# Kernel optimization log

Hardware: AMD Instinct MI355X
Metric: run time of the kernel (lower is better)

Reference implementation:

```python
import jax, jax.numpy as jnp
import numpy as np

K = 16          # neighboursnum
NEG_SLOPE = 0.01  # torch LeakyReLU default
EPS = 1e-5      # torch BatchNorm default


def _bn(x, gamma, beta, axes):
    # BatchNorm in training mode: biased batch stats over `axes`, channel dim = 1
    mu = x.mean(axes, keepdims=True)
    var = x.var(axes, keepdims=True)
    shape = [1] * x.ndim
    shape[1] = -1
    return (x - mu) / jnp.sqrt(var + EPS) * gamma.reshape(shape) + beta.reshape(shape)


def _lrelu(x):
    return jnp.where(x >= 0, x, NEG_SLOPE * x)


def setup_inputs() -> dict:
    key = jax.random.key(0)
    ks = jax.random.split(key, 9)
    B, D, N, O = 4, 64, 4096, 128
    s = 0.05
    return {
        "f_in": jax.random.normal(ks[0], (B, D, N), jnp.float32),
        "w_local": jax.random.normal(ks[1], (O, 2 * D + 1), jnp.float32) * s,
        "g_local": jnp.ones((O,), jnp.float32),
        "b_local": jnp.zeros((O,), jnp.float32),
        "w_sem": jax.random.normal(ks[2], (O, D), jnp.float32) * s,
        "g_sem": jnp.ones((O,), jnp.float32),
        "b_sem": jnp.zeros((O,), jnp.float32),
        "w_full": jax.random.normal(ks[3], (O, 2 * O), jnp.float32) * s,
        "g_full": jnp.ones((O,), jnp.float32),
        "b_full": jnp.zeros((O,), jnp.float32),
        "wq": jax.random.normal(ks[4], (D, D), jnp.float32) * s,
        "bq": jax.random.normal(ks[5], (D,), jnp.float32) * s,
        "wk": jax.random.normal(ks[6], (D, D), jnp.float32) * s,
        "bk": jax.random.normal(ks[7], (D,), jnp.float32) * s,
        "wv": jax.random.normal(ks[8], (D, D), jnp.float32) * s,
        "bv": jax.random.normal(jax.random.fold_in(key, 99), (D,), jnp.float32) * s,
    }


def reference(f_in, w_local, g_local, b_local, w_sem, g_sem, b_sem,
              w_full, g_full, b_full, wq, bq, wk, bk, wv, bv):
    B, D, N = f_in.shape
    # --- knn on feature space: pairwise negative squared distance, topk ---
    xx = jnp.sum(f_in * f_in, axis=1)                       # (B,N)
    inner = jnp.einsum('bdm,bdn->bmn', f_in, f_in)          # (B,N,N)
    pd = -xx[:, :, None] + 2.0 * inner - xx[:, None, :]     # -||xi-xj||^2
    idx = jax.lax.top_k(pd, K)[1]                           # (B,N,K) nearest
    # --- gather graph feature ---
    x_t = jnp.swapaxes(f_in, 1, 2)                          # (B,N,D)
    neigh = x_t[jnp.arange(B)[:, None, None], idx]          # (B,N,K,D)
    central = jnp.broadcast_to(x_t[:, :, None, :], neigh.shape)
    dist = jnp.linalg.norm(neigh - central, axis=3, keepdims=True)  # (B,N,K,1)
    feat = jnp.concatenate([central, neigh, dist], axis=3)  # (B,N,K,2D+1)
    feat = jnp.transpose(feat, (0, 3, 1, 2))                # (B,2D+1,N,K)
    # --- localConv (1x1 conv2d, no bias) + BN2d + LeakyReLU, max over K ---
    intra = _lrelu(_bn(jnp.einsum('oc,bcnk->bonk', w_local, feat),
                       g_local, b_local, (0, 2, 3)))
    intra = intra.max(axis=-1)                              # (B,O,N)
    # --- self-attention over points ---
    q = jnp.einsum('od,bdn->bon', wq, f_in) + bq[None, :, None]
    k = jnp.einsum('od,bdn->bon', wk, f_in) + bk[None, :, None]
    v = jnp.einsum('od,bdn->bon', wv, f_in) + bv[None, :, None]
    scores = jax.nn.softmax(
        jnp.einsum('bdm,bdn->bmn', q, k) / jnp.sqrt(jnp.float32(D)), axis=-1)
    fgt = jnp.einsum('bmn,bdn->bdm', scores, v)             # (B,D,N)
    # --- semConv (1x1 conv1d) + BN1d + LeakyReLU ---
    inter = _lrelu(_bn(jnp.einsum('od,bdn->bon', w_sem, fgt),
                       g_sem, b_sem, (0, 2)))               # (B,O,N)
    # --- fullConv on concat ---
    cat = jnp.concatenate([intra, inter], axis=1)           # (B,2O,N)
    out = _lrelu(_bn(jnp.einsum('oc,bcn->bon', w_full, cat),
                     g_full, b_full, (0, 2)))               # (B,O,N)
    return out
```

## Files before the change

kernel.cpp:

```cpp
#include <hip/hip_runtime.h>
#include <math.h>

constexpr int NB = 4;
constexpr int ND = 64;
constexpr int NNN = 4096;
constexpr int NO = 128;
constexpr int NK = 16;
constexpr float NEG = 0.01f;
constexpr float BN_EPS = 1e-5f;

typedef unsigned short u16;
typedef unsigned int u32;
typedef __attribute__((ext_vector_type(8))) short short8;
typedef __attribute__((ext_vector_type(4))) float floatx4;

constexpr int OFF_XX    = 0;
constexpr int OFF_IDX   = 16384;
constexpr int OFF_D2    = 278528;
constexpr int OFF_Q     = 540672;
constexpr int OFF_K     = 1589248;
constexpr int OFF_V     = 2637824;
constexpr int OFF_FGT   = 3686400;
constexpr int OFF_APRE  = 4734976;
constexpr int OFF_BPRE  = 6832128;
constexpr int OFF_IMAX  = 8929280;
constexpr int OFF_IMIN  = 11026432;
constexpr int OFF_ZSEM  = OFF_Q;
constexpr int OFF_ZFULL = OFF_V;
constexpr int OFF_STATS = 13123584;
constexpr int OFF_COEF  = 13124352;
constexpr int OFF_LINV  = 13125120;

__device__ __forceinline__ u16 f2b(float x) {
  u32 u = __builtin_bit_cast(u32, x);
  u += 0x7fffu + ((u >> 16) & 1u);
  return (u16)(u >> 16);
}

template <int CTRL>
__device__ __forceinline__ float fmax_dpp(float v) {
  int b = __builtin_bit_cast(int, v);
  int s = __builtin_amdgcn_update_dpp(b, b, CTRL, 0xF, 0xF, false);
  return fmaxf(v, __builtin_bit_cast(float, s));
}
__device__ __forceinline__ void pairmax(float av, int ai, float bv, int bi, float& rv, int& ri) {
  bool tk = bv > av;
  rv = tk ? bv : av;
  ri = tk ? bi : ai;
}

__global__ void k_xx(const float* __restrict__ f, float* __restrict__ xx) {
  int gid = blockIdx.x * 256 + threadIdx.x;
  int b = gid >> 12, n = gid & 4095;
  const float* fb = f + b * ND * NNN + n;
  float s = 0.f;
#pragma unroll
  for (int d = 0; d < ND; ++d) { float v = fb[d * NNN]; s += v * v; }
  xx[gid] = s;
}

__global__ __launch_bounds__(256) void k_qkv(const float* __restrict__ f,
    const float* __restrict__ wq, const float* __restrict__ bq,
    const float* __restrict__ wk, const float* __restrict__ bk,
    const float* __restrict__ wv, const float* __restrict__ bv,
    u16* __restrict__ qb, u16* __restrict__ kb, u16* __restrict__ vb) {
  int sel = blockIdx.y;
  const float* W    = (sel == 0) ? wq : (sel == 1) ? wk : wv;
  const float* bias = (sel == 0) ? bq : (sel == 1) ? bk : bv;
  int t = threadIdx.x;
  int lane = t & 63;
  int og = __builtin_amdgcn_readfirstlane(t >> 6);
  int gcol = blockIdx.x * 64 + lane;
  int b = gcol >> 12, n = gcol & 4095;
  const float* fb = f + b * ND * NNN + n;
  float cv[64];
#pragma unroll
  for (int d = 0; d < ND; ++d) cv[d] = fb[d * NNN];
  float acc[16];
#pragma unroll 1
  for (int oi = 0; oi < 16; ++oi) {
    int o = og * 16 + oi;
    const float* wr = W + o * ND;
    float a = bias[o];
#pragma unroll
    for (int d = 0; d < ND; ++d) a += wr[d] * cv[d];
    acc[oi] = a;
  }
  if (sel == 2) {
#pragma unroll
    for (int oi = 0; oi < 16; ++oi)
      vb[(size_t)(b * ND + og * 16 + oi) * NNN + n] = f2b(acc[oi]);
  } else {
    short8 p0, p1;
#pragma unroll
    for (int oi = 0; oi < 8; ++oi) { p0[oi] = (short)f2b(acc[oi]); p1[oi] = (short)f2b(acc[8 + oi]); }
    u16* dst = (sel ? kb : qb) + (size_t)(b * NNN + n) * ND + og * 16;
    *(short8*)dst = p0;
    *(short8*)(dst + 8) = p1;
  }
}

__global__ __launch_bounds__(256, 4) void k_knn(const float* __restrict__ f, const float* __restrict__ xx,
                                                int* __restrict__ tidx, float* __restrict__ td2) {
  __shared__ __align__(16) float fm[ND * 8];
  __shared__ __align__(16) float sl[4 * 2048];
  int t = threadIdx.x;
  int lane = t & 63;
  int w = __builtin_amdgcn_readfirstlane(t >> 6);
  int b = blockIdx.x >> 9;
  int m0 = (blockIdx.x & 511) << 3;
  const float* fb = f + b * ND * NNN;
  { int e = t;       int d = e >> 3, r = e & 7; fm[e] = fb[d * NNN + m0 + r]; }
  { int e = t + 256; int d = e >> 3, r = e & 7; fm[e] = fb[d * NNN + m0 + r]; }
  __syncthreads();
  float lv[2][2];
  int   li[2][2];
#pragma unroll
  for (int h = 0; h < 2; ++h) {
    float acc[64];
#pragma unroll
    for (int i = 0; i < 64; ++i) acc[i] = 0.f;
    for (int d = 0; d < ND; ++d) {
      const float* frow = fb + d * NNN + h * 2048 + 4 * t;
      float4 v0 = *(const float4*)(frow);
      float4 v1 = *(const float4*)(frow + 1024);
      float4 r0 = *(const float4*)&fm[d * 8];
      float4 r1 = *(const float4*)&fm[d * 8 + 4];
      float va0[4] = {v0.x, v0.y, v0.z, v0.w};
      float va1[4] = {v1.x, v1.y, v1.z, v1.w};
      float rr[8]  = {r0.x, r0.y, r0.z, r0.w, r1.x, r1.y, r1.z, r1.w};
#pragma unroll
      for (int c2 = 0; c2 < 4; ++c2)
#pragma unroll
        for (int r = 0; r < 8; ++r) {
          acc[c2 * 8 + r]      += va0[c2] * rr[r];
          acc[32 + c2 * 8 + r] += va1[c2] * rr[r];
        }
    }
    {
      const float* xrow = xx + b * NNN + h * 2048 + 4 * t;
      float4 x0 = *(const float4*)(xrow);
      float4 x1 = *(const float4*)(xrow + 1024);
      float xa0[4] = {x0.x, x0.y, x0.z, x0.w};
      float xa1[4] = {x1.x, x1.y, x1.z, x1.w};
#pragma unroll
      for (int c2 = 0; c2 < 4; ++c2)
#pragma unroll
        for (int r = 0; r < 8; ++r) {
          acc[c2 * 8 + r]      = 2.f * acc[c2 * 8 + r]      - xa0[c2];
          acc[32 + c2 * 8 + r] = 2.f * acc[32 + c2 * 8 + r] - xa1[c2];
        }
    }
#pragma unroll
    for (int s = 0; s < 2; ++s) {
      __syncthreads();
#pragma unroll
      for (int r4 = 0; r4 < 4; ++r4) {
        int r = s * 4 + r4;
#pragma unroll
        for (int jj = 0; jj < 2; ++jj) {
          float4 w4;
          w4.x = acc[jj * 32 + 0 * 8 + r];
          w4.y = acc[jj * 32 + 1 * 8 + r];
          w4.z = acc[jj * 32 + 2 * 8 + r];
          w4.w = acc[jj * 32 + 3 * 8 + r];
          *(float4*)&sl[r4 * 2048 + jj * 1024 + 4 * t] = w4;
        }
      }
      __syncthreads();
      float vals[32];
#pragma unroll
      for (int i = 0; i < 32; ++i) vals[i] = sl[w * 2048 + i * 64 + lane];
      float gv[8]; int gi[8];
#pragma unroll
      for (int g = 0; g < 8; ++g) {
        float v0 = vals[g * 4]; int i0 = (g * 4) * 64 + lane;
#pragma unroll
        for (int k2 = 1; k2 < 4; ++k2)
          pairmax(v0, i0, vals[g * 4 + k2], (g * 4 + k2) * 64 + lane, v0, i0);
        gv[g] = v0; gi[g] = i0;
      }
      float t1v[4]; int t1i[4];
      float t2v[2]; int t2i[2];
      float lvv; int lii;
#pragma unroll
      for (int p = 0; p < 4; ++p) pairmax(gv[2 * p], gi[2 * p], gv[2 * p + 1], gi[2 * p + 1], t1v[p], t1i[p]);
#pragma unroll
      for (int q = 0; q < 2; ++q) pairmax(t1v[2 * q], t1i[2 * q], t1v[2 * q + 1], t1i[2 * q + 1], t2v[q], t2i[q]);
      pairmax(t2v[0], t2i[0], t2v[1], t2i[1], lvv, lii);
      float selv = 0.f; int seli = 0;
#pragma unroll 1
      for (int kx = 0; kx < NK; ++kx) {
        float W = lvv;
        W = fmax_dpp<0xB1>(W);
        W = fmax_dpp<0x4E>(W);
        W = fmax_dpp<0x124>(W);
        W = fmax_dpp<0x128>(W);
        W = fmaxf(W, __shfl_xor(W, 16));
        W = fmaxf(W, __shfl_xor(W, 32));
        unsigned long long mk = __ballot(lvv == W);
        int lw = (int)__ffsll(mk) - 1;
        int wcol = __builtin_amdgcn_readlane(lii, lw);
        if (lane == kx) { selv = W; seli = wcol; }
        int jw = wcol >> 6;
#pragma unroll
        for (int g = 0; g < 8; ++g)
          if (g == (jw >> 2)) {
#pragma unroll
            for (int k2 = 0; k2 < 4; ++k2)
              if (k2 == (jw & 3))
                vals[g * 4 + k2] = (lane == lw) ? -3.0e38f : vals[g * 4 + k2];
            float v0 = vals[g * 4]; int i0 = (g * 4) * 64 + lane;
#pragma unroll
            for (int k2 = 1; k2 < 4; ++k2)
              pairmax(v0, i0, vals[g * 4 + k2], (g * 4 + k2) * 64 + lane, v0, i0);
            gv[g] = v0; gi[g] = i0;
            int p = g >> 1;
            pairmax(gv[2 * p], gi[2 * p], gv[2 * p + 1], gi[2 * p + 1], t1v[p], t1i[p]);
            int q = p >> 1;
            pairmax(t1v[2 * q], t1i[2 * q], t1v[2 * q + 1], t1i[2 * q + 1], t2v[q], t2i[q]);
            pairmax(t2v[0], t2i[0], t2v[1], t2i[1], lvv, lii);
          }
      }
      lv[h][s] = selv; li[h][s] = h * 2048 + seli;
    }
  }
#pragma unroll
  for (int s = 0; s < 2; ++s) {
    int m = m0 + s * 4 + w;
    float xm = xx[b * NNN + m];
    float a   = lv[0][s]; int ai  = li[0][s];
    float bb2 = lv[1][s]; int bi2 = li[1][s];
    int cntB = 0, cntA = 0;
#pragma unroll
    for (int j = 0; j < 16; ++j) {
      float bj = __shfl(bb2, j);
      cntB += (bj > a) ? 1 : 0;
      float aj = __shfl(a, j);
      cntA += (aj >= bb2) ? 1 : 0;
    }
    if (lane < 16) {
      int base = (b * NNN + m) * NK;
      int rA = lane + cntB;
      int rB = lane + cntA;
      if (rA < NK) {
        float dd = xm - a;
        tidx[base + rA] = ai;
        td2[base + rA] = dd > 0.f ? dd : 0.f;
      }
      if (rB < NK) {
        float dd = xm - bb2;
        tidx[base + rB] = bi2;
        td2[base + rB] = dd > 0.f ? dd : 0.f;
      }
    }
  }
}

__global__ __launch_bounds__(256) void k_attn(const u16* __restrict__ qb,
                                              const u16* __restrict__ kb,
                                              const u16* __restrict__ vb,
                                              float* __restrict__ fgt,
                                              float* __restrict__ linv) {
  __shared__ __align__(16) u16 P[16 * 520];
  __shared__ float rsum[4][16];
  int t = threadIdx.x;
  int lane = t & 63;
  int w = __builtin_amdgcn_readfirstlane(t >> 6);
  int quad = lane >> 4;
  int l15 = lane & 15;
  int b = blockIdx.x >> 8;
  int m0 = (blockIdx.x & 255) << 4;
  const u16* qrow = qb + (size_t)(b * NNN + m0 + l15) * ND + quad * 8;
  short8 qa0 = *(const short8*)(qrow);
  short8 qa1 = *(const short8*)(qrow + 32);
  const u16* kbase = kb + (size_t)b * NNN * ND;
  const u16* vrow  = vb + (size_t)(b * ND + w * 16 + l15) * NNN;
  floatx4 c2 = {0.f, 0.f, 0.f, 0.f};
  float rs[4] = {0.f, 0.f, 0.f, 0.f};
#pragma unroll 1
  for (int it = 0; it < 8; ++it) {
    int nchunk = it * 512;
#pragma unroll 1
    for (int ct = 0; ct < 8; ++ct) {
      int cc0 = (w * 8 + ct) * 16;
      const u16* krow = kbase + (size_t)(nchunk + cc0 + l15) * ND + quad * 8;
      short8 kf0 = *(const short8*)(krow);
      short8 kf1 = *(const short8*)(krow + 32);
      floatx4 acc = {0.f, 0.f, 0.f, 0.f};
      acc = __builtin_amdgcn_mfma_f32_16x16x32_bf16(qa0, kf0, acc, 0, 0, 0);
      acc = __builtin_amdgcn_mfma_f32_16x16x32_bf16(qa1, kf1, acc, 0, 0, 0);
      int ccol = cc0 + l15;
#pragma unroll
      for (int r = 0; r < 4; ++r) {
        float e = __expf(acc[r] * 0.125f);
        rs[r] += e;
        P[(quad * 4 + r) * 520 + ccol] = f2b(e);
      }
    }
    __syncthreads();
    const u16* vp = vrow + nchunk + quad * 8;
#pragma unroll
    for (int kk = 0; kk < 16; ++kk) {
      short8 a2 = *(const short8*)&P[l15 * 520 + kk * 32 + quad * 8];
      short8 b2 = *(const short8*)(vp + kk * 32);
      c2 = __builtin_amdgcn_mfma_f32_16x16x32_bf16(a2, b2, c2, 0, 0, 0);
    }
    __syncthreads();
  }
#pragma unroll
  for (int r = 0; r < 4; ++r) {
    float v = rs[r];
    v += __shfl_xor(v, 1); v += __shfl_xor(v, 2);
    v += __shfl_xor(v, 4); v += __shfl_xor(v, 8);
    rs[r] = v;
  }
  if (l15 == 0) {
#pragma unroll
    for (int r = 0; r < 4; ++r) rsum[w][quad * 4 + r] = rs[r];
  }
#pragma unroll
  for (int r = 0; r < 4; ++r)
    fgt[(size_t)(b * NNN + m0 + quad * 4 + r) * ND + w * 16 + l15] = c2[r];
  __syncthreads();
  if (t < 16) {
    float s = rsum[0][t] + rsum[1][t] + rsum[2][t] + rsum[3][t];
    linv[b * NNN + m0 + t] = 1.f / s;
  }
}

__global__ __launch_bounds__(256) void k_ab(const float* __restrict__ f, const float* __restrict__ wl,
                                            float* __restrict__ Apre, float* __restrict__ Bpre) {
  __shared__ float fl[ND * 64];
  int t = threadIdx.x;
  int b = blockIdx.x >> 6;
  int n0 = (blockIdx.x & 63) << 6;
  for (int e = t; e < ND * 64; e += 256) {
    int d = e >> 6, c = e & 63;
    fl[e] = f[b * ND * NNN + d * NNN + n0 + c];
  }
  __syncthreads();
  int lane = t & 63;
  int w = __builtin_amdgcn_readfirstlane(t >> 6);
#pragma unroll 1
  for (int g = 0; g < 8; ++g) {
    float acc[8] = {0, 0, 0, 0, 0, 0, 0, 0};
    int p0 = w * 64 + g * 8;
    for (int d = 0; d < ND; ++d) {
      float fv = fl[d * 64 + lane];
#pragma unroll
      for (int u = 0; u < 8; ++u) {
        int p = p0 + u;
        int o = p & 127, sel = p >> 7;
        acc[u] += wl[o * 129 + sel * 64 + d] * fv;
      }
    }
#pragma unroll
    for (int u = 0; u < 8; ++u) {
      int p = p0 + u;
      int o = p & 127, sel = p >> 7;
      float* outp = sel ? Bpre : Apre;
      outp[(b * NNN + n0 + lane) * NO + o] = acc[u];
    }
  }
}

__global__ __launch_bounds__(128) void k_intra(const float* __restrict__ Apre, const float* __restrict__ Bpre,
                                               const int* __restrict__ tidx, const float* __restrict__ td2,
                                               const float* __restrict__ wl, float* __restrict__ imax,
                                               float* __restrict__ imin, float* __restrict__ stats) {
  __shared__ int sidx[32 * NK];
  __shared__ float sdst[32 * NK];
  int t = threadIdx.x;
  int b = blockIdx.x >> 7;
  int n0 = (blockIdx.x & 127) << 5;
  for (int e = t; e < 32 * NK; e += 128) {
    int base = (b * NNN + n0 + (e >> 4)) * NK + (e & 15);
    sidx[e] = tidx[base];
    sdst[e] = sqrtf(td2[base]);
  }
  __syncthreads();
  int o = t;
  float w128 = wl[o * 129 + 128];
  float ssum = 0.f, ssq = 0.f;
  for (int c = 0; c < 32; ++c) {
    float a = Apre[(b * NNN + n0 + c) * NO + o];
    float mx = -3.4e38f, mn = 3.4e38f;
#pragma unroll
    for (int kx = 0; kx < NK; ++kx) {
      int id = sidx[c * NK + kx];
      float y = a + Bpre[(b * NNN + id) * NO + o] + w128 * sdst[c * NK + kx];
      mx = fmaxf(mx, y); mn = fminf(mn, y);
      ssum += y; ssq += y * y;
    }
    imax[(b * NO + o) * NNN + n0 + c] = mx;
    imin[(b * NO + o) * NNN + n0 + c] = mn;
  }
  atomicAdd(&stats[o], ssum);
  atomicAdd(&stats[NO + o], ssq);
}

__global__ __launch_bounds__(256) void k_sem(const float* __restrict__ fgt, const float* __restrict__ linv,
                                             const float* __restrict__ wsem, float* __restrict__ zsem) {
  __shared__ float fl[64 * 65];
  int t = threadIdx.x;
  int b = blockIdx.x >> 6;
  int n0 = (blockIdx.x & 63) << 6;
  for (int e = t; e < 64 * 64; e += 256) {
    int n = e >> 6, d = e & 63;
    fl[n * 65 + d] = fgt[(size_t)(b * NNN + n0 + n) * ND + d] * linv[b * NNN + n0 + n];
  }
  __syncthreads();
  int lane = t & 63;
  int ob = __builtin_amdgcn_readfirstlane((t >> 6) * 32);
#pragma unroll 1
  for (int g = 0; g < 4; ++g) {
    float acc[8] = {0, 0, 0, 0, 0, 0, 0, 0};
    for (int d = 0; d < ND; ++d) {
      float fv = fl[lane * 65 + d];
#pragma unroll
      for (int u = 0; u < 8; ++u) acc[u] += wsem[(ob + g * 8 + u) * ND + d] * fv;
    }
#pragma unroll
    for (int u = 0; u < 8; ++u)
      zsem[(b * NO + ob + g * 8 + u) * NNN + n0 + lane] = acc[u];
  }
}

__global__ void k_stats(const float* __restrict__ zz, float* __restrict__ sout) {
  int o = blockIdx.x, t = threadIdx.x;
  float s = 0.f, q = 0.f;
  for (int b2 = 0; b2 < NB; ++b2) {
    const float* p = zz + (size_t)(b2 * NO + o) * NNN;
    for (int n = t; n < NNN; n += 256) { float v = p[n]; s += v; q += v * v; }
  }
#pragma unroll
  for (int off = 32; off; off >>= 1) { s += __shfl_down(s, off); q += __shfl_down(q, off); }
  __shared__ float rs[4], rq[4];
  int lane = t & 63, w = t >> 6;
  if (lane == 0) { rs[w] = s; rq[w] = q; }
  __syncthreads();
  if (t == 0) {
    sout[o]      = rs[0] + rs[1] + rs[2] + rs[3];
    sout[NO + o] = rq[0] + rq[1] + rq[2] + rq[3];
  }
}

__global__ void k_fin(const float* __restrict__ stats, const float* __restrict__ g,
                      const float* __restrict__ be, float cnt_inv, float* __restrict__ coef) {
  int o = threadIdx.x;
  float mean = stats[o] * cnt_inv;
  float var = stats[NO + o] * cnt_inv - mean * mean;
  var = var > 0.f ? var : 0.f;
  float a = g[o] * rsqrtf(var + BN_EPS);
  coef[o] = a;
  coef[NO + o] = be[o] - mean * a;
}

__global__ __launch_bounds__(256) void k_full(const float* __restrict__ imax, const float* __restrict__ imin,
                                              const float* __restrict__ zsem, const float* __restrict__ wfull,
                                              const float* __restrict__ coef, float* __restrict__ zfull) {
  __shared__ float fl[2 * NO * 64];
  int t = threadIdx.x;
  int b = blockIdx.x >> 6;
  int n0 = (blockIdx.x & 63) << 6;
  for (int e = t; e < 2 * NO * 64; e += 256) {
    int c = e >> 6, col = e & 63;
    float aa, bb, x;
    if (c < NO) {
      aa = coef[c]; bb = coef[NO + c];
      const float* src = (aa >= 0.f) ? imax : imin;
      x = src[(b * NO + c) * NNN + n0 + col];
    } else {
      int c2 = c - NO;
      aa = coef[2 * NO + c2]; bb = coef[3 * NO + c2];
      x = zsem[(b * NO + c2) * NNN + n0 + col];
    }
    float y = aa * x + bb;
    fl[e] = (y >= 0.f) ? y : NEG * y;
  }
  __syncthreads();
  int lane = t & 63;
  int ob = __builtin_amdgcn_readfirstlane((t >> 6) * 32);
#pragma unroll 1
  for (int g = 0; g < 4; ++g) {
    float acc[8] = {0, 0, 0, 0, 0, 0, 0, 0};
    for (int c = 0; c < 2 * NO; ++c) {
      float fv = fl[c * 64 + lane];
#pragma unroll
      for (int u = 0; u < 8; ++u) acc[u] += wfull[(ob + g * 8 + u) * (2 * NO) + c] * fv;
    }
#pragma unroll
    for (int u = 0; u < 8; ++u)
      zfull[(b * NO + ob + g * 8 + u) * NNN + n0 + lane] = acc[u];
  }
}

__global__ void k_out(const float* __restrict__ zfull, const float* __restrict__ coef,
                      float* __restrict__ out) {
  int gid = blockIdx.x * 256 + threadIdx.x;
  int o = (gid >> 12) & 127;
  float y = coef[o] * zfull[gid] + coef[NO + o];
  out[gid] = (y >= 0.f) ? y : NEG * y;
}

extern "C" void kernel_launch(void* const* d_in, const int* in_sizes, int n_in,
                              void* d_out, int out_size, void* d_ws, size_t ws_size,
                              hipStream_t stream) {
  (void)in_sizes; (void)n_in; (void)out_size; (void)ws_size;
  const float* f       = (const float*)d_in[0];
  const float* w_local = (const float*)d_in[1];
  const float* g_local = (const float*)d_in[2];
  const float* b_local = (const float*)d_in[3];
  const float* w_sem   = (const float*)d_in[4];
  const float* g_sem   = (const float*)d_in[5];
  const float* b_sem   = (const float*)d_in[6];
  const float* w_full  = (const float*)d_in[7];
  const float* g_full  = (const float*)d_in[8];
  const float* b_full  = (const float*)d_in[9];
  const float* wq = (const float*)d_in[10];
  const float* bq = (const float*)d_in[11];
  const float* wk = (const float*)d_in[12];
  const float* bk = (const float*)d_in[13];
  const float* wv = (const float*)d_in[14];
  const float* bv = (const float*)d_in[15];
  float* Wp = (float*)d_ws;
  u16* qb16 = (u16*)(Wp + OFF_Q);
  u16* kb16 = (u16*)(Wp + OFF_K);
  u16* vb16 = (u16*)(Wp + OFF_V);

  hipMemsetAsync(Wp + OFF_STATS, 0, 2 * NO * sizeof(float), stream);
  k_xx  <<<NB * NNN / 256, 256, 0, stream>>>(f, Wp + OFF_XX);
  k_qkv <<<dim3(NB * NNN / 64, 3), 256, 0, stream>>>(f, wq, bq, wk, bk, wv, bv, qb16, kb16, vb16);
  k_knn <<<NB * (NNN / 8), 256, 0, stream>>>(f, Wp + OFF_XX, (int*)(Wp + OFF_IDX), Wp + OFF_D2);
  k_attn<<<NB * (NNN / 16), 256, 0, stream>>>(qb16, kb16, vb16, Wp + OFF_FGT, Wp + OFF_LINV);
  k_ab  <<<NB * (NNN / 64), 256, 0, stream>>>(f, w_local, Wp + OFF_APRE, Wp + OFF_BPRE);
  k_intra<<<NB * (NNN / 32), 128, 0, stream>>>(Wp + OFF_APRE, Wp + OFF_BPRE,
                                               (const int*)(Wp + OFF_IDX), Wp + OFF_D2,
                                               w_local, Wp + OFF_IMAX, Wp + OFF_IMIN, Wp + OFF_STATS);
  k_sem <<<NB * (NNN / 64), 256, 0, stream>>>(Wp + OFF_FGT, Wp + OFF_LINV, w_sem, Wp + OFF_ZSEM);
  k_stats<<<NO, 256, 0, stream>>>(Wp + OFF_ZSEM, Wp + OFF_STATS + 2 * NO);
  k_fin <<<1, NO, 0, stream>>>(Wp + OFF_STATS,          g_local, b_local,
                               1.f / (float)(NB * NNN * NK), Wp + OFF_COEF);
  k_fin <<<1, NO, 0, stream>>>(Wp + OFF_STATS + 2 * NO, g_sem, b_sem,
                               1.f / (float)(NB * NNN), Wp + OFF_COEF + 2 * NO);
  k_full<<<NB * (NNN / 64), 256, 0, stream>>>(Wp + OFF_IMAX, Wp + OFF_IMIN, Wp + OFF_ZSEM,
                                              w_full, Wp + OFF_COEF, Wp + OFF_ZFULL);
  k_stats<<<NO, 256, 0, stream>>>(Wp + OFF_ZFULL, Wp + OFF_STATS + 4 * NO);
  k_fin <<<1, NO, 0, stream>>>(Wp + OFF_STATS + 4 * NO, g_full, b_full,
                               1.f / (float)(NB * NNN), Wp + OFF_COEF + 4 * NO);
  k_out <<<NB * NO * NNN / 256, 256, 0, stream>>>(Wp + OFF_ZFULL, Wp + OFF_COEF + 4 * NO,
                                                  (float*)d_out);
}
```

Baseline: 707.3 us.

## Compute KNN distances with split-bf16 MFMA instead of scalar FP32 FMAs

```diff
diff --git a/kernel.cpp b/kernel.cpp
--- a/kernel.cpp
+++ b/kernel.cpp
@@ -36,6 +36,10 @@
   u += 0x7fffu + ((u >> 16) & 1u);
   return (u16)(u >> 16);
 }
+__device__ __forceinline__ float b2f(u16 h) {
+  u32 u = (u32)h << 16;
+  return __builtin_bit_cast(float, u);
+}
 
 template <int CTRL>
 __device__ __forceinline__ float fmax_dpp(float v) {
@@ -49,13 +53,31 @@
   ri = tk ? bi : ai;
 }
 
-__global__ void k_xx(const float* __restrict__ f, float* __restrict__ xx) {
+__global__ void k_prep(const float* __restrict__ f, float* __restrict__ xx,
+                       u16* __restrict__ fh1, u16* __restrict__ fh2, u16* __restrict__ fh3) {
   int gid = blockIdx.x * 256 + threadIdx.x;
   int b = gid >> 12, n = gid & 4095;
   const float* fb = f + b * ND * NNN + n;
+  u16* p1 = fh1 + (size_t)gid * ND;
+  u16* p2 = fh2 + (size_t)gid * ND;
+  u16* p3 = fh3 + (size_t)gid * ND;
   float s = 0.f;
 #pragma unroll
-  for (int d = 0; d < ND; ++d) { float v = fb[d * NNN]; s += v * v; }
+  for (int c8 = 0; c8 < 8; ++c8) {
+    short8 q1, q2, q3;
+#pragma unroll
+    for (int j = 0; j < 8; ++j) {
+      float x = fb[(c8 * 8 + j) * NNN];
+      s += x * x;
+      u16 h1 = f2b(x);  float r1 = x - b2f(h1);
+      u16 h2 = f2b(r1); float r2 = r1 - b2f(h2);
+      u16 h3 = f2b(r2);
+      q1[j] = (short)h1; q2[j] = (short)h2; q3[j] = (short)h3;
+    }
+    *(short8*)(p1 + c8 * 8) = q1;
+    *(short8*)(p2 + c8 * 8) = q2;
+    *(short8*)(p3 + c8 * 8) = q3;
+  }
   xx[gid] = s;
 }
 
@@ -100,77 +122,68 @@
   }
 }
 
-__global__ __launch_bounds__(256, 4) void k_knn(const float* __restrict__ f, const float* __restrict__ xx,
+__global__ __launch_bounds__(256, 2) void k_knn(const u16* __restrict__ fh1, const u16* __restrict__ fh2,
+                                                const u16* __restrict__ fh3, const float* __restrict__ xx,
                                                 int* __restrict__ tidx, float* __restrict__ td2) {
-  __shared__ __align__(16) float fm[ND * 8];
-  __shared__ __align__(16) float sl[4 * 2048];
+  __shared__ __align__(16) float sl[2048 * 5];
   int t = threadIdx.x;
   int lane = t & 63;
   int w = __builtin_amdgcn_readfirstlane(t >> 6);
-  int b = blockIdx.x >> 9;
-  int m0 = (blockIdx.x & 511) << 3;
-  const float* fb = f + b * ND * NNN;
-  { int e = t;       int d = e >> 3, r = e & 7; fm[e] = fb[d * NNN + m0 + r]; }
-  { int e = t + 256; int d = e >> 3, r = e & 7; fm[e] = fb[d * NNN + m0 + r]; }
-  __syncthreads();
-  float lv[2][2];
-  int   li[2][2];
+  int quad = lane >> 4;
+  int l15 = lane & 15;
+  int b = blockIdx.x >> 8;
+  int m0 = (blockIdx.x & 255) << 4;
+  const u16* abase1 = fh1 + (size_t)(b * NNN + m0 + l15) * ND + quad * 8;
+  const u16* abase2 = fh2 + (size_t)(b * NNN + m0 + l15) * ND + quad * 8;
+  const u16* abase3 = fh3 + (size_t)(b * NNN + m0 + l15) * ND + quad * 8;
+  short8 a1k0 = *(const short8*)(abase1),      a1k1 = *(const short8*)(abase1 + 32);
+  short8 a2k0 = *(const short8*)(abase2),      a2k1 = *(const short8*)(abase2 + 32);
+  short8 a3k0 = *(const short8*)(abase3),      a3k1 = *(const short8*)(abase3 + 32);
+  float lv[2][4]; int li[2][4];
 #pragma unroll
   for (int h = 0; h < 2; ++h) {
-    float acc[64];
-#pragma unroll
-    for (int i = 0; i < 64; ++i) acc[i] = 0.f;
-    for (int d = 0; d < ND; ++d) {
-      const float* frow = fb + d * NNN + h * 2048 + 4 * t;
-      float4 v0 = *(const float4*)(frow);
-      float4 v1 = *(const float4*)(frow + 1024);
-      float4 r0 = *(const float4*)&fm[d * 8];
-      float4 r1 = *(const float4*)&fm[d * 8 + 4];
-      float va0[4] = {v0.x, v0.y, v0.z, v0.w};
-      float va1[4] = {v1.x, v1.y, v1.z, v1.w};
-      float rr[8]  = {r0.x, r0.y, r0.z, r0.w, r1.x, r1.y, r1.z, r1.w};
-#pragma unroll
-      for (int c2 = 0; c2 < 4; ++c2)
-#pragma unroll
-        for (int r = 0; r < 8; ++r) {
-          acc[c2 * 8 + r]      += va0[c2] * rr[r];
-          acc[32 + c2 * 8 + r] += va1[c2] * rr[r];
-        }
-    }
-    {
-      const float* xrow = xx + b * NNN + h * 2048 + 4 * t;
-      float4 x0 = *(const float4*)(xrow);
-      float4 x1 = *(const float4*)(xrow + 1024);
-      float xa0[4] = {x0.x, x0.y, x0.z, x0.w};
-      float xa1[4] = {x1.x, x1.y, x1.z, x1.w};
-#pragma unroll
-      for (int c2 = 0; c2 < 4; ++c2)
-#pragma unroll
-        for (int r = 0; r < 8; ++r) {
-          acc[c2 * 8 + r]      = 2.f * acc[c2 * 8 + r]      - xa0[c2];
-          acc[32 + c2 * 8 + r] = 2.f * acc[32 + c2 * 8 + r] - xa1[c2];
-        }
-    }
-#pragma unroll
-    for (int s = 0; s < 2; ++s) {
+    floatx4 Ct[32];
+#pragma unroll
+    for (int tl = 0; tl < 32; ++tl) {
+      int c0 = h * 2048 + w * 512 + tl * 16;
+      const u16* bb1 = fh1 + (size_t)(b * NNN + c0 + l15) * ND + quad * 8;
+      const u16* bb2 = fh2 + (size_t)(b * NNN + c0 + l15) * ND + quad * 8;
+      const u16* bb3 = fh3 + (size_t)(b * NNN + c0 + l15) * ND + quad * 8;
+      short8 b1k0 = *(const short8*)(bb1), b1k1 = *(const short8*)(bb1 + 32);
+      short8 b2k0 = *(const short8*)(bb2), b2k1 = *(const short8*)(bb2 + 32);
+      short8 b3k0 = *(const short8*)(bb3), b3k1 = *(const short8*)(bb3 + 32);
+      floatx4 acc = {0.f, 0.f, 0.f, 0.f};
+      acc = __builtin_amdgcn_mfma_f32_16x16x32_bf16(a1k0, b1k0, acc, 0, 0, 0);
+      acc = __builtin_amdgcn_mfma_f32_16x16x32_bf16(a1k1, b1k1, acc, 0, 0, 0);
+      acc = __builtin_amdgcn_mfma_f32_16x16x32_bf16(a1k0, b2k0, acc, 0, 0, 0);
+      acc = __builtin_amdgcn_mfma_f32_16x16x32_bf16(a1k1, b2k1, acc, 0, 0, 0);
+      acc = __builtin_amdgcn_mfma_f32_16x16x32_bf16(a2k0, b1k0, acc, 0, 0, 0);
+      acc = __builtin_amdgcn_mfma_f32_16x16x32_bf16(a2k1, b1k1, acc, 0, 0, 0);
+      acc = __builtin_amdgcn_mfma_f32_16x16x32_bf16(a2k0, b2k0, acc, 0, 0, 0);
+      acc = __builtin_amdgcn_mfma_f32_16x16x32_bf16(a2k1, b2k1, acc, 0, 0, 0);
+      acc = __builtin_amdgcn_mfma_f32_16x16x32_bf16(a1k0, b3k0, acc, 0, 0, 0);
+      acc = __builtin_amdgcn_mfma_f32_16x16x32_bf16(a1k1, b3k1, acc, 0, 0, 0);
+      acc = __builtin_amdgcn_mfma_f32_16x16x32_bf16(a3k0, b1k0, acc, 0, 0, 0);
+      acc = __builtin_amdgcn_mfma_f32_16x16x32_bf16(a3k1, b1k1, acc, 0, 0, 0);
+      float xc = xx[b * NNN + c0 + l15];
+#pragma unroll
+      for (int r = 0; r < 4; ++r) Ct[tl][r] = 2.f * acc[r] - xc;
+    }
+#pragma unroll
+    for (int s = 0; s < 4; ++s) {
       __syncthreads();
-#pragma unroll
-      for (int r4 = 0; r4 < 4; ++r4) {
-        int r = s * 4 + r4;
-#pragma unroll
-        for (int jj = 0; jj < 2; ++jj) {
-          float4 w4;
-          w4.x = acc[jj * 32 + 0 * 8 + r];
-          w4.y = acc[jj * 32 + 1 * 8 + r];
-          w4.z = acc[jj * 32 + 2 * 8 + r];
-          w4.w = acc[jj * 32 + 3 * 8 + r];
-          *(float4*)&sl[r4 * 2048 + jj * 1024 + 4 * t] = w4;
+      if (quad == s) {
+#pragma unroll
+        for (int tl = 0; tl < 32; ++tl) {
+          int cc = w * 512 + tl * 16 + l15;
+#pragma unroll
+          for (int r = 0; r < 4; ++r) sl[cc * 5 + r] = Ct[tl][r];
         }
       }
       __syncthreads();
       float vals[32];
 #pragma unroll
-      for (int i = 0; i < 32; ++i) vals[i] = sl[w * 2048 + i * 64 + lane];
+      for (int i = 0; i < 32; ++i) vals[i] = sl[(i * 64 + lane) * 5 + w];
       float gv[8]; int gi[8];
 #pragma unroll
       for (int g = 0; g < 8; ++g) {
@@ -226,7 +239,7 @@
     }
   }
 #pragma unroll
-  for (int s = 0; s < 2; ++s) {
+  for (int s = 0; s < 4; ++s) {
     int m = m0 + s * 4 + w;
     float xm = xx[b * NNN + m];
     float a   = lv[0][s]; int ai  = li[0][s];
@@ -528,11 +541,15 @@
   u16* qb16 = (u16*)(Wp + OFF_Q);
   u16* kb16 = (u16*)(Wp + OFF_K);
   u16* vb16 = (u16*)(Wp + OFF_V);
+  u16* fh1 = (u16*)(Wp + OFF_FGT);
+  u16* fh2 = fh1 + (size_t)NB * NNN * ND;
+  u16* fh3 = fh2 + (size_t)NB * NNN * ND;
 
   hipMemsetAsync(Wp + OFF_STATS, 0, 2 * NO * sizeof(float), stream);
-  k_xx  <<<NB * NNN / 256, 256, 0, stream>>>(f, Wp + OFF_XX);
+  k_prep<<<NB * NNN / 256, 256, 0, stream>>>(f, Wp + OFF_XX, fh1, fh2, fh3);
   k_qkv <<<dim3(NB * NNN / 64, 3), 256, 0, stream>>>(f, wq, bq, wk, bk, wv, bv, qb16, kb16, vb16);
-  k_knn <<<NB * (NNN / 8), 256, 0, stream>>>(f, Wp + OFF_XX, (int*)(Wp + OFF_IDX), Wp + OFF_D2);
+  k_knn <<<NB * (NNN / 16), 256, 0, stream>>>(fh1, fh2, fh3, Wp + OFF_XX,
+                                              (int*)(Wp + OFF_IDX), Wp + OFF_D2);
   k_attn<<<NB * (NNN / 16), 256, 0, stream>>>(qb16, kb16, vb16, Wp + OFF_FGT, Wp + OFF_LINV);
   k_ab  <<<NB * (NNN / 64), 256, 0, stream>>>(f, w_local, Wp + OFF_APRE, Wp + OFF_BPRE);
   k_intra<<<NB * (NNN / 32), 128, 0, stream>>>(Wp + OFF_APRE, Wp + OFF_BPRE,
```

Result: slower. 838.6 us (+18.6%).
